# Kernel tuning notes

Measured on AMD Instinct MI355X. Metric: run time of the kernel, lower is better.

Reference implementation:

```python
import jax, jax.numpy as jnp
import numpy as np

B, N, D = 4, 2048, 1024
H = 16
HD = D // H          # 64
SCALE = 1.0 / HD     # module uses 1/head_dim (NOT 1/sqrt)
NEG = -10000.0       # masked_fill value used by the module
THETA = 10000.0


def setup_inputs() -> dict:
    key = jax.random.key(0)
    ks = jax.random.split(key, 6)
    s = (1.0 / D) ** 0.5  # init_method_normal((1/dim)**0.5)
    return {
        "x": jax.random.normal(ks[0], (B, N, D), jnp.float32),
        "Wq": jax.random.normal(ks[1], (D, D), jnp.float32) * s,
        "Wk": jax.random.normal(ks[2], (D, D), jnp.float32) * s,
        "Wv": jax.random.normal(ks[3], (D, D), jnp.float32) * s,
        "Wo": jax.random.normal(ks[4], (D, D), jnp.float32) * s,
        "bo": jnp.zeros((D,), jnp.float32),
    }


def _rope(t):
    # t: [b, h, n, d]; interleaved-pair rotary (lucidrains rotate_queries_or_keys)
    d, n = t.shape[-1], t.shape[-2]
    inv_freq = 1.0 / (THETA ** (jnp.arange(0, d, 2, dtype=jnp.float32) / d))  # [d/2]
    ang = jnp.arange(n, dtype=jnp.float32)[:, None] * inv_freq[None, :]        # [n, d/2]
    cos = jnp.repeat(jnp.cos(ang), 2, axis=-1)  # [n, d]
    sin = jnp.repeat(jnp.sin(ang), 2, axis=-1)
    x1, x2 = t[..., ::2], t[..., 1::2]
    rot = jnp.stack([-x2, x1], axis=-1).reshape(t.shape)  # rotate_half
    return t * cos + rot * sin


def reference(x, Wq, Wk, Wv, Wo, bo):
    b, n, _ = x.shape
    # QKV projections (no bias; torch Linear: x @ W.T)
    q = (x @ Wq.T).reshape(b, n, H, HD).transpose(0, 2, 1, 3)  # [b,h,n,d]
    k = (x @ Wk.T).reshape(b, n, H, HD).transpose(0, 2, 1, 3)
    v = (x @ Wv.T).reshape(b, n, H, HD).transpose(0, 2, 1, 3)
    # RoPE on q, k
    q = _rope(q)
    k = _rope(k)
    # additive mask: 0 on/below diagonal, -10000 above (causal_mask=True path)
    i = jnp.arange(n)
    add_mask = jnp.where(i[:, None] >= i[None, :], 0.0, NEG).astype(x.dtype)  # [n,n]
    scores = jnp.einsum("bhqd,bhkd->bhqk", q, k) * SCALE + add_mask
    attn = jax.nn.softmax(scores, axis=-1)
    out = jnp.einsum("bhqk,bhkd->bhqd", attn, v)            # [b,h,n,d]
    out = out.transpose(0, 2, 1, 3).reshape(b, n, H * HD)    # [b,n,D]
    return out @ Wo.T + bo
```

## Files before the change

kernel.cpp:

```cpp
#include <hip/hip_runtime.h>
#include <hip/hip_bf16.h>
#include <math.h>

#define B_ 4
#define N_ 2048
#define D_ 1024
#define H_ 16
#define HD_ 64
#define SCALE_ 0.015625f
#define MD_ ((size_t)B_ * N_ * D_)
#define DD_ ((size_t)D_ * D_)
#define BHSZ_ ((size_t)N_ * HD_)
#define QSC_ 0.0225421143f

typedef __hip_bfloat16 bf16;
typedef __attribute__((ext_vector_type(8))) __bf16 bf16x8;
typedef __attribute__((ext_vector_type(4))) float f32x4;
typedef __attribute__((ext_vector_type(16))) float f32x16;

__device__ __forceinline__ float b2f(bf16 x) { return __bfloat162float(x); }
__device__ __forceinline__ bf16 f2b(float x) { return __float2bfloat16(x); }

__device__ __forceinline__ unsigned int pk2(float a, float b) {
  union { bf16 h[2]; unsigned int u; } t;
  t.h[0] = f2b(a); t.h[1] = f2b(b);
  return t.u;
}
__device__ __forceinline__ unsigned int pk2t(float a, float b) {
  return (__float_as_uint(a) >> 16) | (__float_as_uint(b) & 0xffff0000u);
}

__device__ __forceinline__ void gl_lds16(const bf16* g, bf16* l) {
  __builtin_amdgcn_global_load_lds(
      (const __attribute__((address_space(1))) void*)g,
      (__attribute__((address_space(3))) void*)l, 16, 0, 0);
}

__global__ __launch_bounds__(256) void cvt_all(
    const float* __restrict__ x,  const float* __restrict__ wq,
    const float* __restrict__ wk, const float* __restrict__ wv,
    const float* __restrict__ wo, bf16* __restrict__ xb,
    bf16* __restrict__ wb)
{
  const int blk = blockIdx.x;
  const float* s; bf16* d; int i;
  if (blk < 4096)      { s = x;  d = xb;           i = blk; }
  else if (blk < 4608) { s = wq; d = wb;           i = blk - 4096; }
  else if (blk < 5120) { s = wk; d = wb + DD_;     i = blk - 4608; }
  else if (blk < 5632) { s = wv; d = wb + 2 * DD_; i = blk - 5120; }
  else                 { s = wo; d = wb + 3 * DD_; i = blk - 5632; }
  int e = (i * 256 + threadIdx.x) * 8;
  float4 a = *reinterpret_cast<const float4*>(s + e);
  float4 b = *reinterpret_cast<const float4*>(s + e + 4);
  bf16 t[8] = {f2b(a.x), f2b(a.y), f2b(a.z), f2b(a.w),
               f2b(b.x), f2b(b.y), f2b(b.z), f2b(b.w)};
  *reinterpret_cast<int4*>(d + e) = *reinterpret_cast<const int4*>(t);
}

template <int MODE>
__global__ __launch_bounds__(256) void mgemm(
    const bf16* __restrict__ A, const bf16* __restrict__ W,
    const float* __restrict__ bias, void* __restrict__ Cv,
    int M, int N, int K)
{
  __shared__ bf16 As[128 * 32];
  __shared__ bf16 Ws[128 * 32];

  const int tid  = threadIdx.x;
  const int w    = tid >> 6;
  const int lane = tid & 63;
  const int bm   = blockIdx.y * 128;
  const int bn   = blockIdx.x * 128;

  const int wr = (w >> 1) * 64;
  const int wc = (w & 1) * 64;
  const int lm   = lane & 15;
  const int quad = lane >> 4;

  const int srow = lane >> 2;
  const int scol = (lane & 3) * 8;

  f32x4 acc[4][4] = {};

  for (int k0 = 0; k0 < K; k0 += 32) {
#pragma unroll
    for (int cc = 0; cc < 2; ++cc) {
      int c = w * 2 + cc;
      int r = c * 16 + srow;
      gl_lds16(A + (size_t)(bm + r) * K + k0 + scol, &As[c * 512]);
      gl_lds16(W + (size_t)(bn + r) * K + k0 + scol, &Ws[c * 512]);
    }
    __syncthreads();

    bf16x8 af[4], bf_[4];
#pragma unroll
    for (int mi = 0; mi < 4; ++mi)
      af[mi] = *reinterpret_cast<const bf16x8*>(&As[(wr + mi * 16 + lm) * 32 + quad * 8]);
#pragma unroll
    for (int ni = 0; ni < 4; ++ni)
      bf_[ni] = *reinterpret_cast<const bf16x8*>(&Ws[(wc + ni * 16 + lm) * 32 + quad * 8]);

#pragma unroll
    for (int mi = 0; mi < 4; ++mi)
#pragma unroll
      for (int ni = 0; ni < 4; ++ni)
        acc[mi][ni] = __builtin_amdgcn_mfma_f32_16x16x32_bf16(
            af[mi], bf_[ni], acc[mi][ni], 0, 0, 0);
    __syncthreads();
  }

#pragma unroll
  for (int mi = 0; mi < 4; ++mi) {
#pragma unroll
    for (int r = 0; r < 4; ++r) {
      int row = bm + wr + mi * 16 + quad * 4 + r;
#pragma unroll
      for (int ni = 0; ni < 4; ++ni) {
        int col = bn + wc + ni * 16 + lm;
        float v = acc[mi][ni][r];
        if (MODE == 1) {
          v += bias[col];
          reinterpret_cast<float*>(Cv)[(size_t)row * N + col] = v;
        } else {
          int reg = col >> 10;
          int cc  = col & 1023;
          if (reg < 2) {
            reinterpret_cast<bf16*>(Cv)[(size_t)reg * MD_ + (size_t)row * D_ + cc] = f2b(v);
          } else {
            int bb  = row >> 11;
            int key = row & (N_ - 1);
            int hh  = cc >> 6;
            int hd  = cc & 63;
            int t32 = key >> 5, kk = key & 31;
            int hf = kk >> 4, hi = (kk >> 3) & 1, j = kk & 7;
            reinterpret_cast<bf16*>(Cv)[2 * MD_ +
                (size_t)(bb * H_ + hh) * BHSZ_ +
                (size_t)t32 * 2048 + hf * 1024 + hi * 512 + hd * 8 + j] = f2b(v);
          }
        }
      }
    }
  }
}

template <bool ISQ>
__global__ __launch_bounds__(256) void rope_frag(const bf16* __restrict__ src,
                                                 bf16* __restrict__ dst)
{
  const int bn = blockIdx.x;
  const int n = bn & (N_ - 1);
  const int b = bn >> 11;
  const int tid = threadIdx.x;
  const float LN_THETA = 9.210340371976184f;

  const size_t dbase = (size_t)(n >> 5) * 2048 + (size_t)(n & 31) * 8;

#pragma unroll
  for (int rep = 0; rep < 2; ++rep) {
    int p = tid + rep * 256;
    const int h = p >> 5;
    const int i = p & 31;
    float inv = __expf(-((float)(2 * i) / (float)HD_) * LN_THETA);
    float ang = (float)n * inv;
    float sv, cv;
    sincosf(ang, &sv, &cv);

    size_t sidx = (size_t)bn * D_ + h * HD_ + 2 * i;
    float a = b2f(src[sidx]), c = b2f(src[sidx + 1]);
    float r0 = a * cv - c * sv;
    float r1 = c * cv + a * sv;
    if (ISQ) { r0 *= QSC_; r1 *= QSC_; }

    int d = 2 * i;
    int s = d >> 4, hi = (d >> 3) & 1, j = d & 7;
    size_t didx = (size_t)(b * H_ + h) * BHSZ_ + dbase + s * 512 + hi * 256 + j;
    *reinterpret_cast<unsigned int*>(dst + didx) = pk2(r0, r1);
  }
}

__global__ __launch_bounds__(128) void fattn4_kernel(
    const bf16* __restrict__ Qf, const bf16* __restrict__ Kf,
    const bf16* __restrict__ Vf, bf16* __restrict__ O)
{
  __shared__ float Ls[32 * 64];
  __shared__ float Ll[64];

  const int wv   = threadIdx.x >> 6;
  const int lane = threadIdx.x & 63;
  const int blk  = blockIdx.x;
  const int xcd  = blk & 7;
  const int j    = blk >> 3;
  const int qt   = 63 - (j >> 3);
  const int bh   = xcd * 8 + (j & 7);
  const int b    = bh >> 4;
  const int h    = bh & 15;
  const int col  = lane & 31;
  const int hi   = lane >> 5;

  const bf16* Qb = Qf + (size_t)bh * BHSZ_ + (size_t)qt * 2048 + hi * 256 + col * 8;
  const bf16* Kb = Kf + (size_t)bh * BHSZ_ + hi * 256 + col * 8;
  const bf16* Vb = Vf + (size_t)bh * BHSZ_ + hi * 512 + col * 8;

  bf16x8 qb[4];
#pragma unroll
  for (int s = 0; s < 4; ++s)
    qb[s] = *reinterpret_cast<const bf16x8*>(Qb + s * 512);

  f32x16 o0 = {}, o1 = {};
  float lsum = 0.f;

  for (int kst = wv; kst <= qt; kst += 2) {
    const bf16* kp = Kb + (size_t)kst * 2048;
    f32x16 st = {};
#pragma unroll
    for (int s = 0; s < 4; ++s) {
      bf16x8 ka = *reinterpret_cast<const bf16x8*>(kp + s * 512);
      st = __builtin_amdgcn_mfma_f32_32x32x16_bf16(ka, qb[s], st, 0, 0, 0);
    }

    float pe[16];
    if (kst == qt) {
#pragma unroll
      for (int r = 0; r < 16; ++r) {
        int koff = (r & 3) + 8 * (r >> 2) + 4 * hi;
        float e = (koff <= col) ? exp2f(st[r]) : 0.f;
        pe[r] = e; lsum += e;
      }
    } else {
#pragma unroll
      for (int r = 0; r < 16; ++r) {
        float e = exp2f(st[r]);
        pe[r] = e; lsum += e;
      }
    }

    const bf16* vp = Vb + (size_t)kst * 2048;
#pragma unroll
    for (int hf = 0; hf < 2; ++hf) {
      unsigned int a0 = pk2t(pe[8 * hf + 0], pe[8 * hf + 1]);
      unsigned int a1 = pk2t(pe[8 * hf + 2], pe[8 * hf + 3]);
      unsigned int b0 = pk2t(pe[8 * hf + 4], pe[8 * hf + 5]);
      unsigned int b1 = pk2t(pe[8 * hf + 6], pe[8 * hf + 7]);
      unsigned int s0 = hi ? a0 : b0;
      unsigned int s1 = hi ? a1 : b1;
      unsigned int r0 = (unsigned int)__shfl_xor((int)s0, 32);
      unsigned int r1 = (unsigned int)__shfl_xor((int)s1, 32);
      union { uint4 u; bf16x8 v; } pb;
      pb.u.x = hi ? r0 : a0;
      pb.u.y = hi ? r1 : a1;
      pb.u.z = hi ? b0 : r0;
      pb.u.w = hi ? b1 : r1;

      bf16x8 v0 = *reinterpret_cast<const bf16x8*>(vp + hf * 1024);
      bf16x8 v1 = *reinterpret_cast<const bf16x8*>(vp + hf * 1024 + 256);
      o0 = __builtin_amdgcn_mfma_f32_32x32x16_bf16(v0, pb.v, o0, 0, 0, 0);
      o1 = __builtin_amdgcn_mfma_f32_32x32x16_bf16(v1, pb.v, o1, 0, 0, 0);
    }
  }

  if (wv == 1) {
#pragma unroll
    for (int r = 0; r < 16; ++r) {
      Ls[r * 64 + lane]        = o0[r];
      Ls[(16 + r) * 64 + lane] = o1[r];
    }
    Ll[lane] = lsum;
  }
  __syncthreads();
  if (wv == 0) {
    float lt = lsum + Ll[lane];
    lt += __shfl_xor(lt, 32);
    float inv = 1.f / lt;
#pragma unroll
    for (int r = 0; r < 16; ++r) {
      o0[r] = (o0[r] + Ls[r * 64 + lane]) * inv;
      o1[r] = (o1[r] + Ls[(16 + r) * 64 + lane]) * inv;
    }
    bf16* Op = O + ((size_t)(b * N_ + 32 * qt + col)) * D_ + h * HD_;
#pragma unroll
    for (int g = 0; g < 4; ++g) {
      uint2 u;
      u.x = pk2(o0[4 * g + 0], o0[4 * g + 1]);
      u.y = pk2(o0[4 * g + 2], o0[4 * g + 3]);
      *reinterpret_cast<uint2*>(Op + 8 * g + 4 * hi) = u;
      u.x = pk2(o1[4 * g + 0], o1[4 * g + 1]);
      u.y = pk2(o1[4 * g + 2], o1[4 * g + 3]);
      *reinterpret_cast<uint2*>(Op + 32 + 8 * g + 4 * hi) = u;
    }
  }
}

extern "C" void kernel_launch(void* const* d_in, const int* in_sizes, int n_in,
                              void* d_out, int out_size, void* d_ws, size_t ws_size,
                              hipStream_t stream)
{
  const float* x  = (const float*)d_in[0];
  const float* Wq = (const float*)d_in[1];
  const float* Wk = (const float*)d_in[2];
  const float* Wv = (const float*)d_in[3];
  const float* Wo = (const float*)d_in[4];
  const float* bo = (const float*)d_in[5];
  float* out = (float*)d_out;

  const int M = B_ * N_;

  bf16* xb  = (bf16*)d_ws;
  bf16* q   = xb + MD_;
  bf16* k   = q + MD_;
  bf16* vf  = k + MD_;
  bf16* Wqb = vf + MD_;
  bf16* Wob = Wqb + 3 * DD_;

  bf16* Qf = xb;
  bf16* Kf = q;
  bf16* ao = k;

  cvt_all<<<6144, 256, 0, stream>>>(x, Wq, Wk, Wv, Wo, xb, Wqb);

  mgemm<0><<<dim3(24, 64), 256, 0, stream>>>(xb, Wqb, nullptr, q, M, 3 * D_, D_);

  rope_frag<true ><<<M, 256, 0, stream>>>(q, Qf);
  rope_frag<false><<<M, 256, 0, stream>>>(k, Kf);

  fattn4_kernel<<<4096, 128, 0, stream>>>(Qf, Kf, vf, ao);

  mgemm<1><<<dim3(8, 64), 256, 0, stream>>>(ao, Wob, bo, out, M, D_, D_);
}
```

Measured before the change: 297.4 us.

## Write Q/K in fragment layout from GEMM, do RoPE in place, use K=64 tiles

The QKV GEMM epilogue now writes Q and K straight into the per-head fragment layout the attention kernel reads. The two strided RoPE passes become one vectorized in-place kernel over contiguous 16-byte chunks. The GEMM k-step also doubles from 32 to 64 to halve the barrier and loop overhead, at the cost of twice the LDS per block. The GEMM's Q/K stores become scattered across heads, which may reduce write coalescing.

```diff
diff --git a/kernel.cpp b/kernel.cpp
--- a/kernel.cpp
+++ b/kernel.cpp
@@ -63,8 +63,8 @@
     const float* __restrict__ bias, void* __restrict__ Cv,
     int M, int N, int K)
 {
-  __shared__ bf16 As[128 * 32];
-  __shared__ bf16 Ws[128 * 32];
+  __shared__ bf16 As[128 * 64];
+  __shared__ bf16 Ws[128 * 64];
 
   const int tid  = threadIdx.x;
   const int w    = tid >> 6;
@@ -77,35 +77,40 @@
   const int lm   = lane & 15;
   const int quad = lane >> 4;
 
-  const int srow = lane >> 2;
-  const int scol = (lane & 3) * 8;
+  const int srow = lane >> 3;
+  const int scol = (lane & 7) * 8;
 
   f32x4 acc[4][4] = {};
 
-  for (int k0 = 0; k0 < K; k0 += 32) {
-#pragma unroll
-    for (int cc = 0; cc < 2; ++cc) {
-      int c = w * 2 + cc;
-      int r = c * 16 + srow;
+  for (int k0 = 0; k0 < K; k0 += 64) {
+#pragma unroll
+    for (int cc = 0; cc < 4; ++cc) {
+      int c = w * 4 + cc;
+      int r = c * 8 + srow;
       gl_lds16(A + (size_t)(bm + r) * K + k0 + scol, &As[c * 512]);
       gl_lds16(W + (size_t)(bn + r) * K + k0 + scol, &Ws[c * 512]);
     }
     __syncthreads();
 
-    bf16x8 af[4], bf_[4];
-#pragma unroll
-    for (int mi = 0; mi < 4; ++mi)
-      af[mi] = *reinterpret_cast<const bf16x8*>(&As[(wr + mi * 16 + lm) * 32 + quad * 8]);
-#pragma unroll
-    for (int ni = 0; ni < 4; ++ni)
-      bf_[ni] = *reinterpret_cast<const bf16x8*>(&Ws[(wc + ni * 16 + lm) * 32 + quad * 8]);
-
-#pragma unroll
-    for (int mi = 0; mi < 4; ++mi)
+#pragma unroll
+    for (int kh = 0; kh < 2; ++kh) {
+      bf16x8 af[4], bf_[4];
+#pragma unroll
+      for (int mi = 0; mi < 4; ++mi)
+        af[mi] = *reinterpret_cast<const bf16x8*>(
+            &As[(wr + mi * 16 + lm) * 64 + kh * 32 + quad * 8]);
 #pragma unroll
       for (int ni = 0; ni < 4; ++ni)
-        acc[mi][ni] = __builtin_amdgcn_mfma_f32_16x16x32_bf16(
-            af[mi], bf_[ni], acc[mi][ni], 0, 0, 0);
+        bf_[ni] = *reinterpret_cast<const bf16x8*>(
+            &Ws[(wc + ni * 16 + lm) * 64 + kh * 32 + quad * 8]);
+
+#pragma unroll
+      for (int mi = 0; mi < 4; ++mi)
+#pragma unroll
+        for (int ni = 0; ni < 4; ++ni)
+          acc[mi][ni] = __builtin_amdgcn_mfma_f32_16x16x32_bf16(
+              af[mi], bf_[ni], acc[mi][ni], 0, 0, 0);
+    }
     __syncthreads();
   }
 
@@ -124,18 +129,22 @@
         } else {
           int reg = col >> 10;
           int cc  = col & 1023;
+          int bb  = row >> 11;
+          int n   = row & (N_ - 1);
+          int hh  = cc >> 6;
+          int dd  = cc & 63;
           if (reg < 2) {
-            reinterpret_cast<bf16*>(Cv)[(size_t)reg * MD_ + (size_t)row * D_ + cc] = f2b(v);
+            int t32 = n >> 5, m = n & 31;
+            int s = dd >> 4, hb = (dd >> 3) & 1, j = dd & 7;
+            reinterpret_cast<bf16*>(Cv)[(size_t)reg * MD_ +
+                (size_t)(bb * H_ + hh) * BHSZ_ +
+                (size_t)t32 * 2048 + s * 512 + hb * 256 + m * 8 + j] = f2b(v);
           } else {
-            int bb  = row >> 11;
-            int key = row & (N_ - 1);
-            int hh  = cc >> 6;
-            int hd  = cc & 63;
-            int t32 = key >> 5, kk = key & 31;
-            int hf = kk >> 4, hi = (kk >> 3) & 1, j = kk & 7;
+            int t32 = n >> 5, kk = n & 31;
+            int hf = kk >> 4, hb = (kk >> 3) & 1, j = kk & 7;
             reinterpret_cast<bf16*>(Cv)[2 * MD_ +
                 (size_t)(bb * H_ + hh) * BHSZ_ +
-                (size_t)t32 * 2048 + hf * 1024 + hi * 512 + hd * 8 + j] = f2b(v);
+                (size_t)t32 * 2048 + hf * 1024 + hb * 512 + dd * 8 + j] = f2b(v);
           }
         }
       }
@@ -143,39 +152,42 @@
   }
 }
 
-template <bool ISQ>
-__global__ __launch_bounds__(256) void rope_frag(const bf16* __restrict__ src,
-                                                 bf16* __restrict__ dst)
-{
-  const int bn = blockIdx.x;
-  const int n = bn & (N_ - 1);
-  const int b = bn >> 11;
-  const int tid = threadIdx.x;
+__global__ __launch_bounds__(256) void rope_inplace(bf16* __restrict__ qf,
+                                                    bf16* __restrict__ kf)
+{
+  const int half = blockIdx.x >> 12;
+  const int blk  = blockIdx.x & 4095;
+  bf16* base = half ? kf : qf;
   const float LN_THETA = 9.210340371976184f;
 
-  const size_t dbase = (size_t)(n >> 5) * 2048 + (size_t)(n & 31) * 8;
-
-#pragma unroll
-  for (int rep = 0; rep < 2; ++rep) {
-    int p = tid + rep * 256;
-    const int h = p >> 5;
-    const int i = p & 31;
+  size_t e = ((size_t)blk * 256 + threadIdx.x) * 8;
+  int within = (int)(e & (BHSZ_ - 1));
+  int t32 = within >> 11;
+  int rem = within & 2047;
+  int s  = rem >> 9;
+  int hb = (rem >> 8) & 1;
+  int m  = (rem >> 3) & 31;
+  int n  = t32 * 32 + m;
+
+  uint4 raw = *reinterpret_cast<const uint4*>(base + e);
+  unsigned int pr[4] = {raw.x, raw.y, raw.z, raw.w};
+  unsigned int outw[4];
+#pragma unroll
+  for (int p = 0; p < 4; ++p) {
+    int i = s * 8 + hb * 4 + p;
     float inv = __expf(-((float)(2 * i) / (float)HD_) * LN_THETA);
     float ang = (float)n * inv;
     float sv, cv;
     sincosf(ang, &sv, &cv);
-
-    size_t sidx = (size_t)bn * D_ + h * HD_ + 2 * i;
-    float a = b2f(src[sidx]), c = b2f(src[sidx + 1]);
+    float a = b2f(((bf16*)&pr[p])[0]);
+    float c = b2f(((bf16*)&pr[p])[1]);
     float r0 = a * cv - c * sv;
     float r1 = c * cv + a * sv;
-    if (ISQ) { r0 *= QSC_; r1 *= QSC_; }
-
-    int d = 2 * i;
-    int s = d >> 4, hi = (d >> 3) & 1, j = d & 7;
-    size_t didx = (size_t)(b * H_ + h) * BHSZ_ + dbase + s * 512 + hi * 256 + j;
-    *reinterpret_cast<unsigned int*>(dst + didx) = pk2(r0, r1);
-  }
+    if (half == 0) { r0 *= QSC_; r1 *= QSC_; }
+    outw[p] = pk2(r0, r1);
+  }
+  uint4 o = {outw[0], outw[1], outw[2], outw[3]};
+  *reinterpret_cast<uint4*>(base + e) = o;
 }
 
 __global__ __launch_bounds__(128) void fattn4_kernel(
@@ -305,24 +317,20 @@
   const int M = B_ * N_;
 
   bf16* xb  = (bf16*)d_ws;
-  bf16* q   = xb + MD_;
-  bf16* k   = q + MD_;
-  bf16* vf  = k + MD_;
+  bf16* qf  = xb + MD_;
+  bf16* kf  = qf + MD_;
+  bf16* vf  = kf + MD_;
   bf16* Wqb = vf + MD_;
   bf16* Wob = Wqb + 3 * DD_;
-
-  bf16* Qf = xb;
-  bf16* Kf = q;
-  bf16* ao = k;
+  bf16* ao  = xb;
 
   cvt_all<<<6144, 256, 0, stream>>>(x, Wq, Wk, Wv, Wo, xb, Wqb);
 
-  mgemm<0><<<dim3(24, 64), 256, 0, stream>>>(xb, Wqb, nullptr, q, M, 3 * D_, D_);
-
-  rope_frag<true ><<<M, 256, 0, stream>>>(q, Qf);
-  rope_frag<false><<<M, 256, 0, stream>>>(k, Kf);
-
-  fattn4_kernel<<<4096, 128, 0, stream>>>(Qf, Kf, vf, ao);
+  mgemm<0><<<dim3(24, 64), 256, 0, stream>>>(xb, Wqb, nullptr, qf, M, 3 * D_, D_);
+
+  rope_inplace<<<8192, 256, 0, stream>>>(qf, kf);
+
+  fattn4_kernel<<<4096, 128, 0, stream>>>(qf, kf, vf, ao);
 
   mgemm<1><<<dim3(8, 64), 256, 0, stream>>>(ao, Wob, bo, out, M, D_, D_);
 }
```

Measured after the change: 294.6 us. No clear change (-0.9%).
